# Kernel optimization log

Measured on AMD Instinct MI355X. Metric: run time of the kernel, lower is better.

## Reference

```python
import jax, jax.numpy as jnp
import numpy as np

# Equal-time-constant (tau_mem == tau_syn) closed-form spike time, as in
# fastAndDeep utils_spiketime_et: for each causal set of the k earliest input
# spikes, t = tau * (b/a - W0(-c/a * exp(b/a))), with
#   a = sum_k w_k exp(t_k/tau),  b = sum_k w_k t_k exp(t_k/tau) / tau,
#   c = (threshold - leak) * g_leak.
TAU = 1.0
THRESHOLD = 1.0
LEAK = 0.0
G_LEAK = 1.0
INV_E = float(np.exp(-1.0))


def lambertw0(z):
    """Principal-branch Lambert W for z in [-1/e, 0), via Halley iterations."""
    z = jnp.clip(z, -INV_E + 1e-8, -1e-30)
    # branch-point expansion near -1/e, series z(1-z) elsewhere
    w = jnp.where(z < -0.2,
                  -1.0 + jnp.sqrt(2.0 * (1.0 + jnp.e * z)),
                  z * (1.0 - z))
    for _ in range(12):
        ew = jnp.exp(w)
        f = w * ew - z
        wp1 = w + 1.0
        w = w - f / (ew * wp1 - (w + 2.0) * f / (2.0 * wp1))
    return w


def setup_inputs() -> dict:
    key = jax.random.key(0)
    k1, k2 = jax.random.split(key)
    B, NPRE, NPOST = 128, 1024, 256
    # spike times in units of tau, all finite
    input_spikes = jax.random.uniform(k1, (B, NPRE), dtype=jnp.float32)
    # positive weights scaled so many neurons cross threshold
    input_weights = jax.random.uniform(k2, (NPRE, NPOST), dtype=jnp.float32) * 0.1
    return {"input_spikes": input_spikes, "input_weights": input_weights}


def reference(input_spikes, input_weights):
    # input_spikes: (B, NPRE), input_weights: (NPRE, NPOST)
    sort_idx = jnp.argsort(input_spikes, axis=1)                       # (B, NPRE)
    sorted_spikes = jnp.take_along_axis(input_spikes, sort_idx, axis=1)
    sorted_w = input_weights[sort_idx]                                 # (B, NPRE, NPOST)

    inf_mask = jnp.isinf(sorted_spikes)
    s = jnp.where(inf_mask, 0.0, sorted_spikes)[..., None]             # (B, NPRE, 1)
    sw = jnp.where(inf_mask[..., None], 0.0, sorted_w)

    e = jnp.exp(s / TAU)
    a = jnp.cumsum(sw * e, axis=1)                                     # (B, NPRE, NPOST)
    b = jnp.cumsum(sw * s * e, axis=1) / TAU
    c = (THRESHOLD - LEAK) * G_LEAK

    a_safe = jnp.where(jnp.abs(a) > 1e-10, a, 1e-10)
    z = -c / a_safe * jnp.exp(jnp.clip(b / a_safe, -30.0, 30.0))
    valid = (a > 0) & (z >= -INV_E)
    t = TAU * (b / a_safe - lambertw0(z))
    t = jnp.where(valid, t, jnp.inf)                                   # candidate spike times

    # causal-set consistency: spike must be after the k-th sorted input and
    # not later than the (k+1)-th sorted input (last row exempt)
    ss = sorted_spikes[..., None]
    not_after_last = t < ss
    next_spike = jnp.roll(sorted_spikes, -1, axis=1)[..., None]
    not_earlier_than_next = (t > next_spike).at[:, -1, :].set(False)
    t = jnp.where(not_after_last | not_earlier_than_next, jnp.inf, t)

    output_spikes = jnp.min(t, axis=1)                                 # (B, NPOST)
    return output_spikes
```

## Files before the change

kernel.cpp:

```cpp
#include <hip/hip_runtime.h>
#include <math.h>

#define BATCH 128
#define NPRE  1024
#define NPOST 256
#define NJB   128
#define NW    16
#define KPW   16
#define CLEN  256
#define NCHK  4

__device__ __forceinline__ float lambertw0_f(float z) {
    const float INV_E = 0.36787944117144233f;
    float zc = fminf(fmaxf(z, -INV_E + 1e-8f), -1e-30f);
    float w;
    if (zc < -0.2f) {
        w = -1.0f + sqrtf(2.0f * (1.0f + 2.718281828459045f * zc));
    } else {
        w = zc * (1.0f - zc);
    }
#pragma unroll
    for (int it = 0; it < 5; ++it) {
        float ew  = expf(w);
        float f   = w * ew - zc;
        float wp1 = w + 1.0f;
        w = w - f / (ew * wp1 - (w + 2.0f) * f / (2.0f * wp1));
    }
    return w;
}

__global__ __launch_bounds__(1024, 4)
void ttfs_kernel(const float* __restrict__ spikes,
                 const float* __restrict__ Wt,
                 float* __restrict__ out)
{
    __shared__ int    cnt[1024];
    __shared__ int    bstart[1025];
    __shared__ int    wsum[NW];
    __shared__ unsigned long long tmp64[NPRE];
    __shared__ float2 tse[NPRE + 1];
    __shared__ float2 tez[NPRE + 1];
    __shared__ int    sidx[NPRE + 4];
    __shared__ float  pA[NW][NJB + 2], pB[NW][NJB + 2];
    __shared__ int    flags[2];

    const int tid  = threadIdx.x;
    const int lane = tid & 63;
    const int wid  = tid >> 6;
    const int b    = (int)blockIdx.x >> 1;
    const int h    = (int)blockIdx.x & 1;

    {
        float s = spikes[b * NPRE + tid];
        unsigned long long v =
            (((unsigned long long)__float_as_uint(s)) << 32) | (unsigned)tid;
        int bucket = (int)(s * 1024.0f);
        bucket = bucket < 0 ? 0 : (bucket > 1023 ? 1023 : bucket);

        cnt[tid] = 0;
        __syncthreads();
        int arr = atomicAdd(&cnt[bucket], 1);
        __syncthreads();

        int c0 = cnt[tid];
        int x  = c0;
#pragma unroll
        for (int d = 1; d < 64; d <<= 1) {
            int y = __shfl_up(x, d);
            if (lane >= d) x += y;
        }
        if (lane == 63) wsum[wid] = x;
        __syncthreads();
        int ws = (lane < NW) ? wsum[lane] : 0;
#pragma unroll
        for (int d = 1; d < NW; d <<= 1) {
            int y = __shfl_up(ws, d);
            if (lane >= d) ws += y;
        }
        int base = (wid == 0) ? 0 : __shfl(ws, wid - 1);
        bstart[tid] = base + x - c0;
        if (tid == 0) bstart[1024] = NPRE;
        __syncthreads();

        int slot = bstart[bucket] + arr;
        tmp64[slot] = v;
        __syncthreads();

        int st = bstart[bucket], en = bstart[bucket + 1];
        int rk = 0;
        for (int q = st; q < en; ++q) rk += (tmp64[q] < v);
        int fin = st + rk;

        float e = expf(s);
        tse[fin]  = make_float2(s, e);
        tez[fin]  = make_float2(e, s * e);
        sidx[fin] = tid;
    }
    if (tid == 0) {
        tse[NPRE]  = make_float2(INFINITY, INFINITY);
        tez[NPRE]  = make_float2(INFINITY, 0.0f);
        sidx[NPRE] = 0; sidx[NPRE + 1] = 0; sidx[NPRE + 2] = 0; sidx[NPRE + 3] = 0;
    }
    __syncthreads();

    const int j0 = h * NJB;
    const float* __restrict__ Wc0 = Wt + j0 + lane;
    const float* __restrict__ Wc1 = Wt + j0 + 64 + lane;
    const int4* __restrict__ sidx4 = (const int4*)sidx;
    const int kbase = wid * KPW;

    float offA = 0.0f, offB = 0.0f;
    float preA = 0.0f, preB = 0.0f;
    int   baseK = -1;
    bool  doneJ = false;

#define LOADW2(kstart, dst)                                                   \
    {                                                                         \
        int4 Ia = sidx4[((kstart) >> 2) + 0];                                 \
        int4 Ib = sidx4[((kstart) >> 2) + 1];                                 \
        int4 Ic = sidx4[((kstart) >> 2) + 2];                                 \
        int4 Id = sidx4[((kstart) >> 2) + 3];                                 \
        dst[0]  = Wc0[Ia.x * NPOST]; dst[1]  = Wc0[Ia.y * NPOST];             \
        dst[2]  = Wc0[Ia.z * NPOST]; dst[3]  = Wc0[Ia.w * NPOST];             \
        dst[4]  = Wc0[Ib.x * NPOST]; dst[5]  = Wc0[Ib.y * NPOST];             \
        dst[6]  = Wc0[Ib.z * NPOST]; dst[7]  = Wc0[Ib.w * NPOST];             \
        dst[8]  = Wc0[Ic.x * NPOST]; dst[9]  = Wc0[Ic.y * NPOST];             \
        dst[10] = Wc0[Ic.z * NPOST]; dst[11] = Wc0[Ic.w * NPOST];             \
        dst[12] = Wc0[Id.x * NPOST]; dst[13] = Wc0[Id.y * NPOST];             \
        dst[14] = Wc0[Id.z * NPOST]; dst[15] = Wc0[Id.w * NPOST];             \
        dst[16] = Wc1[Ia.x * NPOST]; dst[17] = Wc1[Ia.y * NPOST];             \
        dst[18] = Wc1[Ia.z * NPOST]; dst[19] = Wc1[Ia.w * NPOST];             \
        dst[20] = Wc1[Ib.x * NPOST]; dst[21] = Wc1[Ib.y * NPOST];             \
        dst[22] = Wc1[Ib.z * NPOST]; dst[23] = Wc1[Ib.w * NPOST];             \
        dst[24] = Wc1[Ic.x * NPOST]; dst[25] = Wc1[Ic.y * NPOST];             \
        dst[26] = Wc1[Ic.z * NPOST]; dst[27] = Wc1[Ic.w * NPOST];             \
        dst[28] = Wc1[Id.x * NPOST]; dst[29] = Wc1[Id.y * NPOST];             \
        dst[30] = Wc1[Id.z * NPOST]; dst[31] = Wc1[Id.w * NPOST];             \
    }

    float wv[2 * KPW];
    LOADW2(kbase, wv);

    for (int ch = 0; ch < NCHK; ++ch) {
        const int kk0 = ch * CLEN + kbase;
        float a0 = 0.0f, b0 = 0.0f, a1 = 0.0f, b1 = 0.0f;
#pragma unroll
        for (int i = 0; i < KPW; ++i) {
            float2 t = tez[kk0 + i];
            a0 = fmaf(wv[i],       t.x, a0);
            b0 = fmaf(wv[i],       t.y, b0);
            a1 = fmaf(wv[KPW + i], t.x, a1);
            b1 = fmaf(wv[KPW + i], t.y, b1);
        }
        pA[wid][lane]      = a0; pB[wid][lane]      = b0;
        pA[wid][64 + lane] = a1; pB[wid][64 + lane] = b1;
        __syncthreads();

        if (wid < 2) {
            const int n = (wid << 6) + lane;
#pragma unroll
            for (int w = 0; w < NW; ++w) {
                float nA = offA + pA[w][n];
                float nB = offB + pB[w][n];
                if (!doneJ) {
                    float2 tn = tse[ch * CLEN + (w + 1) * KPW];
                    float gate = fmaf(nA, tn.x, -nB);
                    if (gate >= tn.y) {
                        baseK = ch * CLEN + w * KPW;
                        preA = offA; preB = offB;
                        doneJ = true;
                    }
                }
                offA = nA; offB = nB;
            }
            bool all = __all(doneJ);
            if (lane == 0) flags[wid] = all ? 1 : 0;
        }
        __syncthreads();
        if (flags[0] & flags[1]) break;
        if (ch < NCHK - 1) LOADW2(kk0 + CLEN, wv);
    }

    if (wid < 2) {
        const int n = (wid << 6) + lane;
        const float* __restrict__ Wcol = Wt + j0 + n;
        float result = INFINITY;
        const float INV_E = 0.36787944117144233f;
        if (doneJ) {
            float wl[KPW];
#pragma unroll
            for (int q = 0; q < KPW / 4; ++q) {
                int4 I = sidx4[(baseK >> 2) + q];
                wl[4 * q + 0] = Wcol[I.x * NPOST];
                wl[4 * q + 1] = Wcol[I.y * NPOST];
                wl[4 * q + 2] = Wcol[I.z * NPOST];
                wl[4 * q + 3] = Wcol[I.w * NPOST];
            }
            float A = preA, Bq = preB;
            int fk = -1; float fA = 0.0f, fB = 0.0f;
#pragma unroll
            for (int i = 0; i < KPW; ++i) {
                const int k = baseK + i;
                float2 ez = tez[k];
                A  = fmaf(wl[i], ez.x, A);
                Bq = fmaf(wl[i], ez.y, Bq);
                if (fk < 0) {
                    float2 tn = tse[k + 1];
                    float gate = fmaf(A, tn.x, -Bq);
                    if (gate >= tn.y) { fA = A; fB = Bq; fk = k; }
                }
            }

            if (fk >= 0) {
                float r   = fB / fA;
                float ezz = expf(fminf(fmaxf(r, -30.0f), 30.0f));
                float z   = -ezz / fA;
                bool valid = (fA > 0.0f) && (z >= -INV_E);
                float t = r - lambertw0_f(z);
                bool ok = valid && (t >= tse[fk].x) &&
                          (fk == NPRE - 1 || t <= tse[fk + 1].x);
                if (ok) {
                    result = t;
                } else {
                    float A2 = fA, B2 = fB;
                    for (int k = fk + 1; k < NPRE; ++k) {
                        float w = Wcol[sidx[k] * NPOST];
                        float2 ez2v = tez[k];
                        A2 = fmaf(w, ez2v.x, A2);
                        B2 = fmaf(w, ez2v.y, B2);
                        if (A2 <= 0.0f) continue;
                        float r2  = B2 / A2;
                        float ex2 = expf(fminf(fmaxf(r2, -30.0f), 30.0f));
                        float z2  = -ex2 / A2;
                        if (z2 < -INV_E) continue;
                        float t2 = r2 - lambertw0_f(z2);
                        if (t2 < tse[k].x) continue;
                        if (k < NPRE - 1 && t2 > tse[k + 1].x) continue;
                        result = t2;
                        break;
                    }
                }
            } else {
                float A2 = 0.0f, B2 = 0.0f;
                for (int k = 0; k < NPRE; ++k) {
                    float w = Wcol[sidx[k] * NPOST];
                    float2 ez2v = tez[k];
                    A2 = fmaf(w, ez2v.x, A2);
                    B2 = fmaf(w, ez2v.y, B2);
                    if (A2 <= 0.0f) continue;
                    float r2  = B2 / A2;
                    float ex2 = expf(fminf(fmaxf(r2, -30.0f), 30.0f));
                    float z2  = -ex2 / A2;
                    if (z2 < -INV_E) continue;
                    float t2 = r2 - lambertw0_f(z2);
                    if (t2 < tse[k].x) continue;
                    if (k < NPRE - 1 && t2 > tse[k + 1].x) continue;
                    result = t2;
                    break;
                }
            }
        }
        out[b * NPOST + j0 + n] = result;
    }
}

extern "C" void kernel_launch(void* const* d_in, const int* in_sizes, int n_in,
                              void* d_out, int out_size, void* d_ws, size_t ws_size,
                              hipStream_t stream) {
    const float* spikes  = (const float*)d_in[0];
    const float* weights = (const float*)d_in[1];
    float* outp = (float*)d_out;
    ttfs_kernel<<<dim3(BATCH * 2), dim3(1024), 0, stream>>>(spikes, weights, outp);
}
```

Baseline: 12.87 us.

## Resolve final segment in owning warp using register-resident weights

Stores each neuron's located segment base and prefix sums in shared memory. The warp that already holds the weights for that segment in registers then does the fine-grained scan and the Lambert-W solve, so the 16-element scattered global weight gather is skipped and the work is spread across all warps instead of two. Neurons whose segment fell in an earlier chunk take a fallback path in warps 0–1 that still gathers from global memory. This costs an extra barrier, more shared memory and duplicated code, and divergence moves into many warps.

```diff
diff --git a/kernel.cpp b/kernel.cpp
--- a/kernel.cpp
+++ b/kernel.cpp
@@ -43,6 +43,8 @@
     __shared__ int    sidx[NPRE + 4];
     __shared__ float  pA[NW][NJB + 2], pB[NW][NJB + 2];
     __shared__ int    flags[2];
+    __shared__ int    rbaseK[NJB];
+    __shared__ float  rpreA[NJB], rpreB[NJB];
 
     const int tid  = threadIdx.x;
     const int lane = tid & 63;
@@ -141,7 +143,8 @@
     float wv[2 * KPW];
     LOADW2(kbase, wv);
 
-    for (int ch = 0; ch < NCHK; ++ch) {
+    int ch = 0;
+    for (; ch < NCHK; ++ch) {
         const int kk0 = ch * CLEN + kbase;
         float a0 = 0.0f, b0 = 0.0f, a1 = 0.0f, b1 = 0.0f;
 #pragma unroll
@@ -180,54 +183,74 @@
         if (flags[0] & flags[1]) break;
         if (ch < NCHK - 1) LOADW2(kk0 + CLEN, wv);
     }
+    const int regCh = (ch < NCHK) ? ch : NCHK - 1;
 
     if (wid < 2) {
         const int n = (wid << 6) + lane;
-        const float* __restrict__ Wcol = Wt + j0 + n;
-        float result = INFINITY;
-        const float INV_E = 0.36787944117144233f;
-        if (doneJ) {
-            float wl[KPW];
-#pragma unroll
-            for (int q = 0; q < KPW / 4; ++q) {
-                int4 I = sidx4[(baseK >> 2) + q];
-                wl[4 * q + 0] = Wcol[I.x * NPOST];
-                wl[4 * q + 1] = Wcol[I.y * NPOST];
-                wl[4 * q + 2] = Wcol[I.z * NPOST];
-                wl[4 * q + 3] = Wcol[I.w * NPOST];
-            }
-            float A = preA, Bq = preB;
-            int fk = -1; float fA = 0.0f, fB = 0.0f;
-#pragma unroll
-            for (int i = 0; i < KPW; ++i) {
-                const int k = baseK + i;
-                float2 ez = tez[k];
-                A  = fmaf(wl[i], ez.x, A);
-                Bq = fmaf(wl[i], ez.y, Bq);
-                if (fk < 0) {
-                    float2 tn = tse[k + 1];
-                    float gate = fmaf(A, tn.x, -Bq);
-                    if (gate >= tn.y) { fA = A; fB = Bq; fk = k; }
-                }
-            }
-
-            if (fk >= 0) {
-                float r   = fB / fA;
-                float ezz = expf(fminf(fmaxf(r, -30.0f), 30.0f));
-                float z   = -ezz / fA;
-                bool valid = (fA > 0.0f) && (z >= -INV_E);
-                float t = r - lambertw0_f(z);
-                bool ok = valid && (t >= tse[fk].x) &&
-                          (fk == NPRE - 1 || t <= tse[fk + 1].x);
-                if (ok) {
-                    result = t;
+        rbaseK[n] = baseK; rpreA[n] = preA; rpreB[n] = preB;
+    }
+    __syncthreads();
+
+    {
+        const int myBase = regCh * CLEN + kbase;
+#pragma unroll
+        for (int half = 0; half < 2; ++half) {
+            const int n = (half << 6) + lane;
+            if (rbaseK[n] == myBase) {
+                const float* __restrict__ Wcol = Wt + j0 + n;
+                const float INV_E = 0.36787944117144233f;
+                float result = INFINITY;
+                float A = rpreA[n], Bq = rpreB[n];
+                int fk = -1; float fA = 0.0f, fB = 0.0f;
+#pragma unroll
+                for (int i = 0; i < KPW; ++i) {
+                    const int k = myBase + i;
+                    float2 ez = tez[k];
+                    float wgt = wv[half * KPW + i];
+                    A  = fmaf(wgt, ez.x, A);
+                    Bq = fmaf(wgt, ez.y, Bq);
+                    if (fk < 0) {
+                        float2 tn = tse[k + 1];
+                        float gate = fmaf(A, tn.x, -Bq);
+                        if (gate >= tn.y) { fA = A; fB = Bq; fk = k; }
+                    }
+                }
+                if (fk >= 0) {
+                    float r   = fB / fA;
+                    float ezz = expf(fminf(fmaxf(r, -30.0f), 30.0f));
+                    float z   = -ezz / fA;
+                    bool valid = (fA > 0.0f) && (z >= -INV_E);
+                    float t = r - lambertw0_f(z);
+                    bool ok = valid && (t >= tse[fk].x) &&
+                              (fk == NPRE - 1 || t <= tse[fk + 1].x);
+                    if (ok) {
+                        result = t;
+                    } else {
+                        float A2 = fA, B2 = fB;
+                        for (int k = fk + 1; k < NPRE; ++k) {
+                            float w = Wcol[sidx[k] * NPOST];
+                            float2 ezv = tez[k];
+                            A2 = fmaf(w, ezv.x, A2);
+                            B2 = fmaf(w, ezv.y, B2);
+                            if (A2 <= 0.0f) continue;
+                            float r2  = B2 / A2;
+                            float ex2 = expf(fminf(fmaxf(r2, -30.0f), 30.0f));
+                            float z2  = -ex2 / A2;
+                            if (z2 < -INV_E) continue;
+                            float t2 = r2 - lambertw0_f(z2);
+                            if (t2 < tse[k].x) continue;
+                            if (k < NPRE - 1 && t2 > tse[k + 1].x) continue;
+                            result = t2;
+                            break;
+                        }
+                    }
                 } else {
-                    float A2 = fA, B2 = fB;
-                    for (int k = fk + 1; k < NPRE; ++k) {
+                    float A2 = 0.0f, B2 = 0.0f;
+                    for (int k = 0; k < NPRE; ++k) {
                         float w = Wcol[sidx[k] * NPOST];
-                        float2 ez2v = tez[k];
-                        A2 = fmaf(w, ez2v.x, A2);
-                        B2 = fmaf(w, ez2v.y, B2);
+                        float2 ezv = tez[k];
+                        A2 = fmaf(w, ezv.x, A2);
+                        B2 = fmaf(w, ezv.y, B2);
                         if (A2 <= 0.0f) continue;
                         float r2  = B2 / A2;
                         float ex2 = expf(fminf(fmaxf(r2, -30.0f), 30.0f));
@@ -240,27 +263,93 @@
                         break;
                     }
                 }
-            } else {
-                float A2 = 0.0f, B2 = 0.0f;
-                for (int k = 0; k < NPRE; ++k) {
-                    float w = Wcol[sidx[k] * NPOST];
-                    float2 ez2v = tez[k];
-                    A2 = fmaf(w, ez2v.x, A2);
-                    B2 = fmaf(w, ez2v.y, B2);
-                    if (A2 <= 0.0f) continue;
-                    float r2  = B2 / A2;
-                    float ex2 = expf(fminf(fmaxf(r2, -30.0f), 30.0f));
-                    float z2  = -ex2 / A2;
-                    if (z2 < -INV_E) continue;
-                    float t2 = r2 - lambertw0_f(z2);
-                    if (t2 < tse[k].x) continue;
-                    if (k < NPRE - 1 && t2 > tse[k + 1].x) continue;
-                    result = t2;
-                    break;
-                }
+                out[b * NPOST + j0 + n] = result;
             }
         }
-        out[b * NPOST + j0 + n] = result;
+    }
+
+    if (wid < 2) {
+        const int n = (wid << 6) + lane;
+        const int bK = rbaseK[n];
+        if (bK < regCh * CLEN) {
+            const float* __restrict__ Wcol = Wt + j0 + n;
+            float result = INFINITY;
+            const float INV_E = 0.36787944117144233f;
+            if (bK >= 0) {
+                float wl[KPW];
+#pragma unroll
+                for (int q = 0; q < KPW / 4; ++q) {
+                    int4 I = sidx4[(bK >> 2) + q];
+                    wl[4 * q + 0] = Wcol[I.x * NPOST];
+                    wl[4 * q + 1] = Wcol[I.y * NPOST];
+                    wl[4 * q + 2] = Wcol[I.z * NPOST];
+                    wl[4 * q + 3] = Wcol[I.w * NPOST];
+                }
+                float A = rpreA[n], Bq = rpreB[n];
+                int fk = -1; float fA = 0.0f, fB = 0.0f;
+#pragma unroll
+                for (int i = 0; i < KPW; ++i) {
+                    const int k = bK + i;
+                    float2 ez = tez[k];
+                    A  = fmaf(wl[i], ez.x, A);
+                    Bq = fmaf(wl[i], ez.y, Bq);
+                    if (fk < 0) {
+                        float2 tn = tse[k + 1];
+                        float gate = fmaf(A, tn.x, -Bq);
+                        if (gate >= tn.y) { fA = A; fB = Bq; fk = k; }
+                    }
+                }
+                if (fk >= 0) {
+                    float r   = fB / fA;
+                    float ezz = expf(fminf(fmaxf(r, -30.0f), 30.0f));
+                    float z   = -ezz / fA;
+                    bool valid = (fA > 0.0f) && (z >= -INV_E);
+                    float t = r - lambertw0_f(z);
+                    bool ok = valid && (t >= tse[fk].x) &&
+                              (fk == NPRE - 1 || t <= tse[fk + 1].x);
+                    if (ok) {
+                        result = t;
+                    } else {
+                        float A2 = fA, B2 = fB;
+                        for (int k = fk + 1; k < NPRE; ++k) {
+                            float w = Wcol[sidx[k] * NPOST];
+                            float2 ezv = tez[k];
+                            A2 = fmaf(w, ezv.x, A2);
+                            B2 = fmaf(w, ezv.y, B2);
+                            if (A2 <= 0.0f) continue;
+                            float r2  = B2 / A2;
+                            float ex2 = expf(fminf(fmaxf(r2, -30.0f), 30.0f));
+                            float z2  = -ex2 / A2;
+                            if (z2 < -INV_E) continue;
+                            float t2 = r2 - lambertw0_f(z2);
+                            if (t2 < tse[k].x) continue;
+                            if (k < NPRE - 1 && t2 > tse[k + 1].x) continue;
+                            result = t2;
+                            break;
+                        }
+                    }
+                } else {
+                    float A2 = 0.0f, B2 = 0.0f;
+                    for (int k = 0; k < NPRE; ++k) {
+                        float w = Wcol[sidx[k] * NPOST];
+                        float2 ezv = tez[k];
+                        A2 = fmaf(w, ezv.x, A2);
+                        B2 = fmaf(w, ezv.y, B2);
+                        if (A2 <= 0.0f) continue;
+                        float r2  = B2 / A2;
+                        float ex2 = expf(fminf(fmaxf(r2, -30.0f), 30.0f));
+                        float z2  = -ex2 / A2;
+                        if (z2 < -INV_E) continue;
+                        float t2 = r2 - lambertw0_f(z2);
+                        if (t2 < tse[k].x) continue;
+                        if (k < NPRE - 1 && t2 > tse[k + 1].x) continue;
+                        result = t2;
+                        break;
+                    }
+                }
+            }
+            out[b * NPOST + j0 + n] = result;
+        }
     }
 }
 
```

Result: slower. 14.98 us (+16.4%).
